# Performance work log

Measured on AMD Instinct MI355X. Metric: run time of the kernel, lower is better.

Reference implementation:

```python
import jax, jax.numpy as jnp
import numpy as np

H = 32; W = 32; KH = 3; KW = 3; NH = 8; DIM = 256; MLP_DIM = 1024; B = 4; T_FULL = 9
DH = DIM // NH
NEG = -1e9


def layernorm(x, g, b):
    m = jnp.mean(x, axis=-1, keepdims=True)
    v = jnp.var(x, axis=-1, keepdims=True)
    return (x - m) / jnp.sqrt(v + 1e-5) * g + b


def rope(x):
    # x: (B, NH, T, DH); split-half rotary position embedding
    T, dh = x.shape[-2], x.shape[-1]
    inv = 1.0 / (10000.0 ** (jnp.arange(0, dh, 2, dtype=jnp.float32) / dh))
    ang = jnp.arange(T, dtype=jnp.float32)[:, None] * inv  # (T, dh/2)
    cos, sin = jnp.cos(ang), jnp.sin(ang)
    x1, x2 = jnp.split(x, 2, axis=-1)
    return jnp.concatenate([x1 * cos - x2 * sin, x1 * sin + x2 * cos], axis=-1)


def setup_inputs() -> dict:
    key = jax.random.key(0)
    ks = jax.random.split(key, 16)
    def w(i, shp):
        return jax.random.normal(ks[i], shp, jnp.float32) * 0.02
    d = {
        'query': jax.random.normal(ks[0], (B, T_FULL, H * W, DIM), jnp.float32),
        'spatial_mask': jnp.zeros((1,), bool),          # unused by forward (module builds its own)
        'temporal_mask': jnp.zeros((T_FULL, T_FULL), bool),
        'sln_g': jnp.ones((DIM,), jnp.float32), 'sln_b': jnp.zeros((DIM,), jnp.float32),
        's_wq': w(1, (DIM, DIM)), 's_bq': jnp.zeros((DIM,), jnp.float32),
        's_wk': w(2, (DIM, DIM)), 's_bk': jnp.zeros((DIM,), jnp.float32),
        's_wv': w(3, (DIM, DIM)), 's_bv': jnp.zeros((DIM,), jnp.float32),
        's_wo': w(4, (DIM, DIM)), 's_bo': jnp.zeros((DIM,), jnp.float32),
        'tln_g': jnp.ones((DIM,), jnp.float32), 'tln_b': jnp.zeros((DIM,), jnp.float32),
        't_wq': w(5, (DIM, DIM)), 't_bq': jnp.zeros((DIM,), jnp.float32),
        't_wk': w(6, (DIM, DIM)), 't_bk': jnp.zeros((DIM,), jnp.float32),
        't_wv': w(7, (DIM, DIM)), 't_bv': jnp.zeros((DIM,), jnp.float32),
        't_wo': w(8, (DIM, DIM)), 't_bo': jnp.zeros((DIM,), jnp.float32),
        'mln_g': jnp.ones((DIM,), jnp.float32), 'mln_b': jnp.zeros((DIM,), jnp.float32),
        'w1': w(9, (DIM, MLP_DIM)), 'b1': jnp.zeros((MLP_DIM,), jnp.float32),
        'w2': w(10, (MLP_DIM, DIM)), 'b2': jnp.zeros((DIM,), jnp.float32),
    }
    return d


def _forward(query, temporal_mask, sln_g, sln_b, s_wq, s_bq, s_wk, s_bk, s_wv, s_bv, s_wo, s_bo,
             tln_g, tln_b, t_wq, t_bq, t_wk, t_bk, t_wv, t_bv, t_wo, t_bo,
             mln_g, mln_b, w1, b1, w2, b2):
    Bq, Tq, HWn, Dn = query.shape
    T = Tq - 1
    size = KH * KW
    scale = 1.0 / jnp.sqrt(jnp.float32(DH))

    # ---- spatial windowed attention on frames [:-1] (unfold -> per-window 1x9 attention) ----
    visual = query[:, :T].reshape(Bq * T, H, W, Dn)
    pad = jnp.pad(visual, ((0, 0), (KH // 2, KH // 2), (KW // 2, KW // 2), (0, 0)))
    neigh = jnp.stack([pad[:, i:i + H, j:j + W, :] for i in range(KH) for j in range(KW)], axis=1)
    neigh = neigh.reshape(Bq * T, size, HWn, Dn).transpose(0, 2, 1, 3)  # (BT, HW, size, D)
    onep = jnp.pad(jnp.ones((H, W), jnp.float32), ((KH // 2, KH // 2), (KW // 2, KW // 2)))
    valid = jnp.stack([onep[i:i + H, j:j + W] for i in range(KH) for j in range(KW)], axis=0)
    pad_mask = (valid.reshape(size, HWn).T == 0)  # (HW, size) True where neighbor from padding

    vis = visual.reshape(Bq * T, HWn, 1, Dn)
    vis_n = layernorm(vis, sln_g, sln_b)
    nei_n = layernorm(neigh, sln_g, sln_b)
    q = (vis_n @ s_wq + s_bq).reshape(Bq * T, HWn, 1, NH, DH)
    k = (nei_n @ s_wk + s_bk).reshape(Bq * T, HWn, size, NH, DH)
    v = (nei_n @ s_wv + s_bv).reshape(Bq * T, HWn, size, NH, DH)
    scores = jnp.einsum('bnqhd,bnkhd->bnhqk', q, k) * scale
    scores = jnp.where(pad_mask[None, :, None, None, :], NEG, scores)
    attn = jax.nn.softmax(scores, axis=-1)
    o = jnp.einsum('bnhqk,bnkhd->bnqhd', attn, v).reshape(Bq * T, HWn, 1, Dn)
    o = o @ s_wo + s_bo
    x_sp = (o + vis).reshape(Bq, T, HWn, Dn)

    x = jnp.concatenate([x_sp, query[:, -1:]], axis=1)  # (B, T_, HW, D)

    # ---- temporal RoPE attention per spatial location ----
    xt = x.transpose(0, 2, 1, 3).reshape(Bq * HWn, Tq, Dn)
    xn = layernorm(xt, tln_g, tln_b)
    qt = rope((xn @ t_wq + t_bq).reshape(-1, Tq, NH, DH).transpose(0, 2, 1, 3))
    kt = rope((xn @ t_wk + t_bk).reshape(-1, Tq, NH, DH).transpose(0, 2, 1, 3))
    vt = (xn @ t_wv + t_bv).reshape(-1, Tq, NH, DH).transpose(0, 2, 1, 3)
    sc = jnp.einsum('bhqd,bhkd->bhqk', qt, kt) * scale
    sc = jnp.where(temporal_mask[None, None, :, :], NEG, sc)
    at = jax.nn.softmax(sc, axis=-1)
    ot = jnp.einsum('bhqk,bhkd->bhqd', at, vt).transpose(0, 2, 1, 3).reshape(-1, Tq, Dn)
    xt = (ot @ t_wo + t_bo) + xt
    x = xt.reshape(Bq, HWn, Tq, Dn).transpose(0, 2, 1, 3)

    # CLS frame (t=0): average over spatial positions, broadcast back
    avg_cls = jnp.mean(x[:, 0], axis=1, keepdims=True)  # (B, 1, D)
    x = x.at[:, 0].set(jnp.broadcast_to(avg_cls, (Bq, HWn, Dn)))

    # ---- MLP block ----
    xm = layernorm(x, mln_g, mln_b)
    xm = jax.nn.gelu(xm @ w1 + b1, approximate=False) @ w2 + b2
    return xm + x


def reference(query, spatial_mask, temporal_mask, sln_g, sln_b, s_wq, s_bq, s_wk, s_bk, s_wv, s_bv, s_wo, s_bo, tln_g, tln_b, t_wq, t_bq, t_wk, t_bk, t_wv, t_bv, t_wo, t_bo, mln_g, mln_b, w1, b1, w2, b2):
    # spatial_mask is accepted but unused by the original forward (it rebuilds its own)
    return _forward(query, temporal_mask, sln_g, sln_b, s_wq, s_bq, s_wk, s_bk, s_wv, s_bv, s_wo, s_bo,
                    tln_g, tln_b, t_wq, t_bq, t_wk, t_bk, t_wv, t_bv, t_wo, t_bo,
                    mln_g, mln_b, w1, b1, w2, b2)
```

## Files before the change

### kernel.cpp

```cpp
#include <hip/hip_runtime.h>
#include <math.h>

#define TQ_  9

typedef unsigned int   u32;
typedef unsigned short ushort_t;
typedef short bf16x8 __attribute__((ext_vector_type(8)));
typedef float f32x4  __attribute__((ext_vector_type(4)));

__device__ __forceinline__ float bs2f(ushort_t s) {
  return __uint_as_float(((u32)s) << 16);
}
__device__ __forceinline__ ushort_t f2bs(float x) {
  u32 u = __float_as_uint(x);
  u32 r = (u + 0x7FFFu + ((u >> 16) & 1u)) >> 16;
  return (ushort_t)r;
}

struct TPA { const float* s[10]; ushort_t* d[10]; int K[10]; int N[10]; int pm[10]; };

__global__ __launch_bounds__(256)
void pack_all_kernel(TPA p) {
  int z = blockIdx.z;
  int K = p.K[z], N = p.N[z];
  int bn = blockIdx.x << 5, bk = blockIdx.y << 5;
  if (bn >= N || bk >= K) return;
  const float* W = p.s[z];
  ushort_t* pk = p.d[z];
  int pm = p.pm[z];
  __shared__ float t[32][33];
  int tid = threadIdx.x;
  int tx = tid & 31, ty = tid >> 5;
  #pragma unroll
  for (int r = 0; r < 4; ++r)
    t[ty + (r << 3)][tx] = W[(long)(bk + ty + (r << 3)) * N + bn + tx];
  __syncthreads();
  if (tid < 128) {
    int jl = tid >> 6, q = (tid >> 4) & 3, ln = tid & 15;
    int j = (bn >> 4) + jl, kk = bk >> 5;
    int colsrc = pm ? ((ln & 7) + (jl << 3) + ((ln & 8) << 1))
                    : ((jl << 4) + ln);
    long G = (((long)j * (K >> 5) + kk) << 6) + (q << 4) + ln;
    bf16x8 ov;
    #pragma unroll
    for (int e = 0; e < 8; ++e)
      ov[e] = (short)f2bs(t[(q << 3) + e][colsrc]);
    *(bf16x8*)(pk + (G << 3)) = ov;
  }
}

struct BC6 { const float* b[6]; };
__global__ __launch_bounds__(768)
void bias_concat_kernel(BC6 p, float* __restrict__ dst) {
  int z = blockIdx.x, n = threadIdx.x;
  int w = n >> 8, q = n & 255;
  int psrc = q;
  if (w < 2)
    psrc = (q & 0xE0) | (q & 7) | (((q >> 4) & 1) << 3) | (((q >> 3) & 1) << 4);
  dst[z * 768 + n] = p.b[z * 3 + w][psrc];
}

__global__ __launch_bounds__(256)
void ln_norm_kernel(const float* __restrict__ src, int spatial,
                    const float* __restrict__ g, const float* __restrict__ b,
                    ushort_t* __restrict__ dst) {
  int row = blockIdx.x * 4 + (threadIdx.x >> 6);
  int lane = threadIdx.x & 63;
  long srow = row;
  if (spatial) {
    int bq = row >> 13, r = row & 8191;
    srow = ((long)(bq * TQ_ + (r >> 10)) << 10) + (r & 1023);
  }
  float4 v = ((const float4*)(src + srow * 256))[lane];
  float s  = v.x + v.y + v.z + v.w;
  float s2 = v.x * v.x + v.y * v.y + v.z * v.z + v.w * v.w;
  #pragma unroll
  for (int m = 32; m; m >>= 1) {
    s  += __shfl_xor(s,  m, 64);
    s2 += __shfl_xor(s2, m, 64);
  }
  float mean = s * (1.f / 256.f);
  float rstd = rsqrtf(s2 * (1.f / 256.f) - mean * mean + 1e-5f);
  float4 gv = ((const float4*)g)[lane];
  float4 bv = ((const float4*)b)[lane];
  ushort_t o[4];
  o[0] = f2bs((v.x - mean) * rstd * gv.x + bv.x);
  o[1] = f2bs((v.y - mean) * rstd * gv.y + bv.y);
  o[2] = f2bs((v.z - mean) * rstd * gv.z + bv.z);
  o[3] = f2bs((v.w - mean) * rstd * gv.w + bv.w);
  u32 lo = (u32)o[0] | ((u32)o[1] << 16);
  u32 hi = (u32)o[2] | ((u32)o[3] << 16);
  uint2 pk; pk.x = lo; pk.y = hi;
  *(uint2*)(dst + (long)row * 256 + lane * 4) = pk;
}

template<int K>
__global__ __launch_bounds__(256, 4)
void wgemm_kernel(const ushort_t* __restrict__ A, int lda,
                  const ushort_t* __restrict__ packW,
                  const float* __restrict__ bias, const float* __restrict__ resid,
                  float* __restrict__ Cf, ushort_t* __restrict__ Cb,
                  int N, int NBq, int resid_mode, int out_mode, int act, int rope) {
  constexpr int K32 = K / 32;
  constexpr int AD = (K32 >= 4) ? 4 : K32;
  constexpr int BD = 2;

  int tid = threadIdx.x;
  int wv = tid >> 6, lane = tid & 63;
  int ln = lane & 15, q4 = lane >> 4;

  int gid = blockIdx.x;
  int g = gid >> 5, r = gid & 31;
  int nq = (r >> 3) + ((g % NBq) << 2);
  int mb = ((g / NBq) << 3) + (r & 7);
  int m0 = mb << 7, n0 = nq << 6;

  const ushort_t* Ap = A + (long)(m0 + (wv << 5) + ln) * lda + (q4 << 3);
  long a16 = (long)lda << 4;
  const ushort_t* Bp = packW + (((long)(nq << 2) * K32) << 9) + (lane << 3);

  bf16x8 xr[AD][2];
  bf16x8 wr[BD][4];
  #pragma unroll
  for (int d = 0; d < BD; ++d)
    #pragma unroll
    for (int j = 0; j < 4; ++j)
      wr[d][j] = *(const bf16x8*)(Bp + (((long)j * K32 + d) << 9));
  #pragma unroll
  for (int d = 0; d < AD; ++d) {
    xr[d][0] = *(const bf16x8*)(Ap + d * 32);
    xr[d][1] = *(const bf16x8*)(Ap + a16 + d * 32);
  }

  f32x4 acc[2][4];
  #pragma unroll
  for (int i = 0; i < 2; ++i)
    #pragma unroll
    for (int j = 0; j < 4; ++j) acc[i][j] = 0.f;

  #pragma unroll
  for (int kk = 0; kk < K32; ++kk) {
    #pragma unroll
    for (int i = 0; i < 2; ++i)
      #pragma unroll
      for (int j = 0; j < 4; ++j)
        acc[i][j] = __builtin_amdgcn_mfma_f32_16x16x32_bf16(
            wr[kk % BD][j], xr[kk % AD][i], acc[i][j], 0, 0, 0);
    if (kk + AD < K32) {
      xr[kk % AD][0] = *(const bf16x8*)(Ap + (kk + AD) * 32);
      xr[kk % AD][1] = *(const bf16x8*)(Ap + a16 + (kk + AD) * 32);
    }
    if (kk + BD < K32) {
      #pragma unroll
      for (int j = 0; j < 4; ++j)
        wr[kk % BD][j] = *(const bf16x8*)(Bp + (((long)j * K32 + kk + BD) << 9));
    }
    __builtin_amdgcn_sched_barrier(0);
  }

  float4 bj[4];
  #pragma unroll
  for (int j = 0; j < 4; ++j)
    bj[j] = *(const float4*)(bias + n0 + (j << 4) + (q4 << 2));

  float cs_c[2][4], cs_s[2][4];
  if (rope) {
    int t = (m0 >> 10) % TQ_;
    #pragma unroll
    for (int p = 0; p < 2; ++p)
      #pragma unroll
      for (int r2 = 0; r2 < 4; ++r2) {
        float d = (float)(((q4 & 1) << 2) + r2 + (p << 3));
        float ang = (float)t * exp2f(d * -0.8304820237218406f);
        cs_c[p][r2] = cosf(ang);
        float s = sinf(ang);
        cs_s[p][r2] = (q4 & 2) ? s : -s;
      }
  }

  #pragma unroll
  for (int i = 0; i < 2; ++i) {
    int m = m0 + (wv << 5) + (i << 4) + ln;
    long orow = m;
    if (out_mode == 1 || resid_mode == 2) {
      int bq = m >> 13, rr = m & 8191;
      orow = ((long)(bq * TQ_ + (rr >> 10)) << 10) + (rr & 1023);
    }
    #pragma unroll
    for (int j = 0; j < 4; ++j) {
      int n = n0 + (j << 4) + (q4 << 2);
      float v[4];
      #pragma unroll
      for (int r2 = 0; r2 < 4; ++r2) v[r2] = acc[i][j][r2] + bj[j][r2];
      if (rope && ((nq << 2) + j) < 32) {
        #pragma unroll
        for (int r2 = 0; r2 < 4; ++r2) {
          float other = __shfl_xor(v[r2], 32, 64);
          v[r2] = v[r2] * cs_c[j & 1][r2] + other * cs_s[j & 1][r2];
        }
      }
      if (act) {
        #pragma unroll
        for (int r2 = 0; r2 < 4; ++r2) {
          float x = v[r2];
          v[r2] = 0.5f * x * (1.f + erff(x * 0.70710678118654752f));
        }
      }
      if (resid_mode == 1) {
        float4 rv = *(const float4*)(resid + (long)m * 256 + n);
        v[0] += rv.x; v[1] += rv.y; v[2] += rv.z; v[3] += rv.w;
      } else if (resid_mode == 2) {
        float4 rv = *(const float4*)(resid + orow * 256 + n);
        v[0] += rv.x; v[1] += rv.y; v[2] += rv.z; v[3] += rv.w;
      }
      if (out_mode == 2) {
        uint2 pk;
        pk.x = (u32)f2bs(v[0]) | ((u32)f2bs(v[1]) << 16);
        pk.y = (u32)f2bs(v[2]) | ((u32)f2bs(v[3]) << 16);
        *(uint2*)(Cb + (long)m * N + n) = pk;
      } else {
        float4 o4; o4.x = v[0]; o4.y = v[1]; o4.z = v[2]; o4.w = v[3];
        if (out_mode == 1) *(float4*)(Cf + orow * 256 + n) = o4;
        else               *(float4*)(Cf + (long)m * N + n) = o4;
      }
    }
  }
}

__global__ __launch_bounds__(256)
void spatial_attn_kernel(ushort_t* __restrict__ qkv) {
  int gid = blockIdx.x * 256 + threadIdx.x;
  int head = gid & 7, pixel = gid >> 3;
  int pix = pixel & 1023, bt = pixel >> 10;
  int y = pix >> 5, x = pix & 31;
  long rb = (long)bt << 10;
  const float scale = 0.17677669529663687f;

  float qf[32];
  long qoff = (long)pixel * 768 + head * 32;
  #pragma unroll
  for (int i = 0; i < 4; ++i) {
    bf16x8 t = *(const bf16x8*)(qkv + qoff + i * 8);
    #pragma unroll
    for (int e = 0; e < 8; ++e) qf[i * 8 + e] = bs2f((ushort_t)t[e]);
  }

  float s[9];
  bool val[9];
  #pragma unroll
  for (int n = 0; n < 9; ++n) {
    int yy = y + n / 3 - 1, xx = x + n % 3 - 1;
    bool ok = ((unsigned)yy < 32u) & ((unsigned)xx < 32u);
    val[n] = ok;
    float d = 0.f;
    if (ok) {
      long ko = (rb + (yy << 5) + xx) * 768 + 256 + head * 32;
      #pragma unroll
      for (int i = 0; i < 4; ++i) {
        bf16x8 t = *(const bf16x8*)(qkv + ko + i * 8);
        #pragma unroll
        for (int e = 0; e < 8; ++e) d += qf[i * 8 + e] * bs2f((ushort_t)t[e]);
      }
    }
    s[n] = d * scale;
  }
  float mx = -1e30f;
  #pragma unroll
  for (int n = 0; n < 9; ++n) if (val[n]) mx = fmaxf(mx, s[n]);
  float sum = 0.f;
  #pragma unroll
  for (int n = 0; n < 9; ++n) { s[n] = val[n] ? __expf(s[n] - mx) : 0.f; sum += s[n]; }
  float inv = 1.f / sum;

  float o[32];
  #pragma unroll
  for (int i = 0; i < 32; ++i) o[i] = 0.f;
  #pragma unroll
  for (int n = 0; n < 9; ++n) {
    if (val[n]) {
      int yy = y + n / 3 - 1, xx = x + n % 3 - 1;
      long vo = (rb + (yy << 5) + xx) * 768 + 512 + head * 32;
      #pragma unroll
      for (int i = 0; i < 4; ++i) {
        bf16x8 t = *(const bf16x8*)(qkv + vo + i * 8);
        #pragma unroll
        for (int e = 0; e < 8; ++e) o[i * 8 + e] += s[n] * bs2f((ushort_t)t[e]);
      }
    }
  }
  #pragma unroll
  for (int i = 0; i < 4; ++i) {
    bf16x8 t;
    #pragma unroll
    for (int e = 0; e < 8; ++e) t[e] = (short)f2bs(o[i * 8 + e] * inv);
    *(bf16x8*)(qkv + qoff + i * 8) = t;
  }
}

__global__ __launch_bounds__(256)
void temporal_attn_kernel(ushort_t* __restrict__ qkv) {
  int tid = threadIdx.x;
  int head = tid & 7, hwi = tid >> 3;
  int bi = blockIdx.x;
  int tq = bi >> 7;
  int rest = bi & 127;
  int b = rest >> 5, hwg = rest & 31;
  int hw = (hwg << 5) + hwi;
  long base = (long)(b * TQ_) * 1024 + hw;
  const float scale = 0.17677669529663687f;

  float qf[32];
  long qoff = (base + (long)tq * 1024) * 768 + head * 32;
  #pragma unroll
  for (int i = 0; i < 4; ++i) {
    bf16x8 t = *(const bf16x8*)(qkv + qoff + i * 8);
    #pragma unroll
    for (int e = 0; e < 8; ++e) qf[i * 8 + e] = bs2f((ushort_t)t[e]);
  }
  float s[9];
  #pragma unroll
  for (int tk = 0; tk < 9; ++tk) {
    long ko = (base + (long)tk * 1024) * 768 + 256 + head * 32;
    float d = 0.f;
    #pragma unroll
    for (int i = 0; i < 4; ++i) {
      bf16x8 t = *(const bf16x8*)(qkv + ko + i * 8);
      #pragma unroll
      for (int e = 0; e < 8; ++e) d += qf[i * 8 + e] * bs2f((ushort_t)t[e]);
    }
    s[tk] = d * scale;
  }
  float mx = s[0];
  #pragma unroll
  for (int tk = 1; tk < 9; ++tk) mx = fmaxf(mx, s[tk]);
  float sum = 0.f;
  #pragma unroll
  for (int tk = 0; tk < 9; ++tk) { s[tk] = __expf(s[tk] - mx); sum += s[tk]; }
  float inv = 1.f / sum;

  float o[32];
  #pragma unroll
  for (int i = 0; i < 32; ++i) o[i] = 0.f;
  #pragma unroll
  for (int tk = 0; tk < 9; ++tk) {
    long vo = (base + (long)tk * 1024) * 768 + 512 + head * 32;
    #pragma unroll
    for (int i = 0; i < 4; ++i) {
      bf16x8 t = *(const bf16x8*)(qkv + vo + i * 8);
      #pragma unroll
      for (int e = 0; e < 8; ++e) o[i * 8 + e] += s[tk] * bs2f((ushort_t)t[e]);
    }
  }
  #pragma unroll
  for (int i = 0; i < 4; ++i) {
    bf16x8 t;
    #pragma unroll
    for (int e = 0; e < 8; ++e) t[e] = (short)f2bs(o[i * 8 + e] * inv);
    *(bf16x8*)(qkv + qoff + i * 8) = t;
  }
}

__global__ __launch_bounds__(256)
void copy_frame8_kernel(const float* __restrict__ qy, float* __restrict__ x) {
  long i = (long)blockIdx.x * 256 + threadIdx.x;
  int b = (int)(i >> 18);
  long rem = i & ((1L << 18) - 1);
  long gi = ((long)(b * TQ_ + 8) << 18) + rem;
  x[gi] = qy[gi];
}

__global__ __launch_bounds__(256)
void cls_sum_kernel(const float* __restrict__ x, float* __restrict__ partial) {
  int b = blockIdx.x >> 5, ch = blockIdx.x & 31;
  int d = threadIdx.x;
  long base = ((long)(b * TQ_) * 1024 + ch * 32) * 256 + d;
  float s = 0.f;
  for (int r = 0; r < 32; ++r) s += x[base + (long)r * 256];
  partial[(long)blockIdx.x * 256 + d] = s;
}

__global__ __launch_bounds__(256)
void cls_bcast_kernel(float* __restrict__ x, const float* __restrict__ partial) {
  int b = blockIdx.x >> 3, seg = blockIdx.x & 7;
  int d = threadIdx.x;
  float s = 0.f;
  for (int j = 0; j < 32; ++j) s += partial[(long)(b * 32 + j) * 256 + d];
  s *= (1.f / 1024.f);
  long base = ((long)(b * TQ_) * 1024 + seg * 128) * 256 + d;
  for (int r = 0; r < 128; ++r) x[base + (long)r * 256] = s;
}

extern "C" void kernel_launch(void* const* d_in, const int* in_sizes, int n_in,
                              void* d_out, int out_size, void* d_ws, size_t ws_size,
                              hipStream_t stream) {
  (void)in_sizes; (void)n_in; (void)out_size; (void)ws_size;
  const float* query = (const float*)d_in[0];
  const float* sln_g = (const float*)d_in[3];
  const float* sln_b = (const float*)d_in[4];
  const float* s_wq  = (const float*)d_in[5];
  const float* s_bq  = (const float*)d_in[6];
  const float* s_wk  = (const float*)d_in[7];
  const float* s_bk  = (const float*)d_in[8];
  const float* s_wv  = (const float*)d_in[9];
  const float* s_bv  = (const float*)d_in[10];
  const float* s_wo  = (const float*)d_in[11];
  const float* s_bo  = (const float*)d_in[12];
  const float* tln_g = (const float*)d_in[13];
  const float* tln_b = (const float*)d_in[14];
  const float* t_wq  = (const float*)d_in[15];
  const float* t_bq  = (const float*)d_in[16];
  const float* t_wk  = (const float*)d_in[17];
  const float* t_bk  = (const float*)d_in[18];
  const float* t_wv  = (const float*)d_in[19];
  const float* t_bv  = (const float*)d_in[20];
  const float* t_wo  = (const float*)d_in[21];
  const float* t_bo  = (const float*)d_in[22];
  const float* mln_g = (const float*)d_in[23];
  const float* mln_b = (const float*)d_in[24];
  const float* w1    = (const float*)d_in[25];
  const float* b1    = (const float*)d_in[26];
  const float* w2    = (const float*)d_in[27];
  const float* b2    = (const float*)d_in[28];
  float* out = (float*)d_out;

  const long RB = 36864L * 256;
  ushort_t* XA  = (ushort_t*)d_ws;
  ushort_t* QKV = XA + RB;
  float*    P4  = (float*)(QKV + 3 * RB);
  ushort_t* wt  = (ushort_t*)(P4 + RB);
  float* bias2  = (float*)(wt + 1048576);
  float* clsp   = bias2 + 1536;
  ushort_t* hid = QKV;

  ushort_t* pk_sqkv = wt;
  ushort_t* pk_tqkv = wt + 196608;
  ushort_t* pk_swo  = wt + 393216;
  ushort_t* pk_two  = wt + 458752;
  ushort_t* pk_w1   = wt + 524288;
  ushort_t* pk_w2   = wt + 786432;

  TPA tp;
  tp.s[0] = s_wq; tp.d[0] = pk_sqkv;          tp.K[0] = 256;  tp.N[0] = 256;  tp.pm[0] = 1;
  tp.s[1] = s_wk; tp.d[1] = pk_sqkv + 65536;  tp.K[1] = 256;  tp.N[1] = 256;  tp.pm[1] = 1;
  tp.s[2] = s_wv; tp.d[2] = pk_sqkv + 131072; tp.K[2] = 256;  tp.N[2] = 256;  tp.pm[2] = 0;
  tp.s[3] = t_wq; tp.d[3] = pk_tqkv;          tp.K[3] = 256;  tp.N[3] = 256;  tp.pm[3] = 1;
  tp.s[4] = t_wk; tp.d[4] = pk_tqkv + 65536;  tp.K[4] = 256;  tp.N[4] = 256;  tp.pm[4] = 1;
  tp.s[5] = t_wv; tp.d[5] = pk_tqkv + 131072; tp.K[5] = 256;  tp.N[5] = 256;  tp.pm[5] = 0;
  tp.s[6] = s_wo; tp.d[6] = pk_swo;           tp.K[6] = 256;  tp.N[6] = 256;  tp.pm[6] = 0;
  tp.s[7] = t_wo; tp.d[7] = pk_two;           tp.K[7] = 256;  tp.N[7] = 256;  tp.pm[7] = 0;
  tp.s[8] = w1;   tp.d[8] = pk_w1;            tp.K[8] = 256;  tp.N[8] = 1024; tp.pm[8] = 0;
  tp.s[9] = w2;   tp.d[9] = pk_w2;            tp.K[9] = 1024; tp.N[9] = 256;  tp.pm[9] = 0;
  pack_all_kernel<<<dim3(32, 32, 10), 256, 0, stream>>>(tp);
  BC6 bc;
  bc.b[0] = s_bq; bc.b[1] = s_bk; bc.b[2] = s_bv;
  bc.b[3] = t_bq; bc.b[4] = t_bk; bc.b[5] = t_bv;
  bias_concat_kernel<<<2, 768, 0, stream>>>(bc, bias2);

  #define WGEMM(KV, Ap, ldav, Wp, bi, rs, CF, CB, M, N, rm, om, ac, rp)     \
    wgemm_kernel<KV><<<dim3(((M) / 128) * ((N) / 64)), 256, 0, stream>>>(   \
        Ap, ldav, Wp, bi, rs, CF, CB, N, (N) / 256, rm, om, ac, rp)

  ln_norm_kernel<<<8192, 256, 0, stream>>>(query, 1, sln_g, sln_b, XA);
  WGEMM(256, XA, 256, pk_sqkv, bias2, nullptr, nullptr, QKV,
        32768, 768, 0, 2, 0, 0);
  spatial_attn_kernel<<<1024, 256, 0, stream>>>(QKV);
  WGEMM(256, QKV, 768, pk_swo, s_bo, query, P4, nullptr,
        32768, 256, 2, 1, 0, 0);
  copy_frame8_kernel<<<4096, 256, 0, stream>>>(query, P4);

  ln_norm_kernel<<<9216, 256, 0, stream>>>(P4, 0, tln_g, tln_b, XA);
  WGEMM(256, XA, 256, pk_tqkv, bias2 + 768, nullptr, nullptr, QKV,
        36864, 768, 0, 2, 0, 1);
  temporal_attn_kernel<<<1152, 256, 0, stream>>>(QKV);
  WGEMM(256, QKV, 768, pk_two, t_bo, P4, out, nullptr,
        36864, 256, 1, 0, 0, 0);

  cls_sum_kernel<<<128, 256, 0, stream>>>(out, clsp);
  cls_bcast_kernel<<<32, 256, 0, stream>>>(out, clsp);

  ln_norm_kernel<<<9216, 256, 0, stream>>>(out, 0, mln_g, mln_b, XA);
  WGEMM(256, XA, 256, pk_w1, b1, nullptr, nullptr, hid,
        36864, 1024, 0, 2, 1, 0);
  WGEMM(1024, hid, 1024, pk_w2, b2, out, out, nullptr,
        36864, 256, 1, 0, 0, 0);
  #undef WGEMM
}
```

Before: 527.1 us.

## Fuse MLP LayerNorm, W1 GEMM, GELU and W2 GEMM into one kernel

Replaces the separate LayerNorm, W1 GEMM (writing a 36864x1024 bf16 hidden buffer) and W2 GEMM with a single kernel. Each 64-thread block handles 32 rows: it normalizes them into LDS, computes the hidden activations in 64-column chunks with GELU, and immediately accumulates them into the W2 output using MFMA. This removes the global round trip of the large hidden tensor. In exchange, each single-wave block streams all of W1 and W2 from global or cache without LDS reuse, and occupancy is low at 1152 one-wave blocks.

```diff
diff --git a/kernel.cpp b/kernel.cpp
--- a/kernel.cpp
+++ b/kernel.cpp
@@ -223,6 +223,148 @@
         if (out_mode == 1) *(float4*)(Cf + orow * 256 + n) = o4;
         else               *(float4*)(Cf + (long)m * N + n) = o4;
       }
+    }
+  }
+}
+
+__device__ __forceinline__ int xl_off(int row, int col) {
+  return (row << 8) + (((((col >> 3) + row) & 31)) << 3) + (col & 7);
+}
+__device__ __forceinline__ int hl_off(int row, int col) {
+  return (row << 6) + (((((col >> 3) + row) & 7)) << 3) + (col & 7);
+}
+
+__global__ __launch_bounds__(64)
+void mlp_fused_kernel(float* xio,
+                      const ushort_t* __restrict__ W1p,
+                      const float* __restrict__ b1,
+                      const ushort_t* __restrict__ W2p,
+                      const float* __restrict__ b2,
+                      const float* __restrict__ g,
+                      const float* __restrict__ be) {
+  __shared__ ushort_t XL[8192];
+  __shared__ ushort_t HL[2048];
+  int lane = threadIdx.x;
+  int ln = lane & 15, q4 = lane >> 4;
+  int m0 = blockIdx.x << 5;
+
+  float mean[2], rstd[2];
+  #pragma unroll
+  for (int i = 0; i < 2; ++i) {
+    const float* xr = xio + (long)(m0 + (i << 4) + ln) * 256 + (q4 << 3);
+    float s = 0.f, s2 = 0.f;
+    #pragma unroll
+    for (int ks = 0; ks < 8; ++ks) {
+      float4 a = *(const float4*)(xr + (ks << 5));
+      float4 b = *(const float4*)(xr + (ks << 5) + 4);
+      s  += a.x + a.y + a.z + a.w + b.x + b.y + b.z + b.w;
+      s2 += a.x*a.x + a.y*a.y + a.z*a.z + a.w*a.w
+          + b.x*b.x + b.y*b.y + b.z*b.z + b.w*b.w;
+    }
+    s  += __shfl_xor(s,  16, 64);  s  += __shfl_xor(s,  32, 64);
+    s2 += __shfl_xor(s2, 16, 64);  s2 += __shfl_xor(s2, 32, 64);
+    mean[i] = s * (1.f / 256.f);
+    rstd[i] = rsqrtf(s2 * (1.f / 256.f) - mean[i] * mean[i] + 1e-5f);
+  }
+
+  #pragma unroll
+  for (int ks = 0; ks < 8; ++ks) {
+    int col = (q4 << 3) + (ks << 5);
+    float4 ga = *(const float4*)(g + col);
+    float4 gb = *(const float4*)(g + col + 4);
+    float4 ba = *(const float4*)(be + col);
+    float4 bb = *(const float4*)(be + col + 4);
+    #pragma unroll
+    for (int i = 0; i < 2; ++i) {
+      const float* xr = xio + (long)(m0 + (i << 4) + ln) * 256 + col;
+      float4 a = *(const float4*)(xr);
+      float4 b = *(const float4*)(xr + 4);
+      float m_ = mean[i], r_ = rstd[i];
+      u32 w0 = (u32)f2bs((a.x - m_) * r_ * ga.x + ba.x)
+             | ((u32)f2bs((a.y - m_) * r_ * ga.y + ba.y) << 16);
+      u32 w1_ = (u32)f2bs((a.z - m_) * r_ * ga.z + ba.z)
+             | ((u32)f2bs((a.w - m_) * r_ * ga.w + ba.w) << 16);
+      u32 w2_ = (u32)f2bs((b.x - m_) * r_ * gb.x + bb.x)
+             | ((u32)f2bs((b.y - m_) * r_ * gb.y + bb.y) << 16);
+      u32 w3 = (u32)f2bs((b.z - m_) * r_ * gb.z + bb.z)
+             | ((u32)f2bs((b.w - m_) * r_ * gb.w + bb.w) << 16);
+      uint4 pk; pk.x = w0; pk.y = w1_; pk.z = w2_; pk.w = w3;
+      *(uint4*)&XL[xl_off((i << 4) + ln, col)] = pk;
+    }
+  }
+
+  f32x4 acc[2][16];
+  #pragma unroll
+  for (int i = 0; i < 2; ++i)
+    #pragma unroll
+    for (int jo = 0; jo < 16; ++jo) acc[i][jo] = 0.f;
+
+  #pragma unroll 1
+  for (int c = 0; c < 16; ++c) {
+    f32x4 h[2][4];
+    #pragma unroll
+    for (int i = 0; i < 2; ++i)
+      #pragma unroll
+      for (int jj = 0; jj < 4; ++jj) h[i][jj] = 0.f;
+
+    #pragma unroll
+    for (int ks = 0; ks < 8; ++ks) {
+      int col = (q4 << 3) + (ks << 5);
+      bf16x8 xf0 = *(const bf16x8*)&XL[xl_off(ln, col)];
+      bf16x8 xf1 = *(const bf16x8*)&XL[xl_off(16 + ln, col)];
+      #pragma unroll
+      for (int jj = 0; jj < 4; ++jj) {
+        bf16x8 wf = *(const bf16x8*)(W1p +
+            (((long)((c << 2) + jj) * 8 + ks) << 9) + (lane << 3));
+        h[0][jj] = __builtin_amdgcn_mfma_f32_16x16x32_bf16(wf, xf0, h[0][jj], 0, 0, 0);
+        h[1][jj] = __builtin_amdgcn_mfma_f32_16x16x32_bf16(wf, xf1, h[1][jj], 0, 0, 0);
+      }
+    }
+    #pragma unroll
+    for (int jj = 0; jj < 4; ++jj) {
+      float4 b1v = *(const float4*)(b1 + (c << 6) + (jj << 4) + (q4 << 2));
+      #pragma unroll
+      for (int i = 0; i < 2; ++i) {
+        float v[4];
+        v[0] = h[i][jj][0] + b1v.x;  v[1] = h[i][jj][1] + b1v.y;
+        v[2] = h[i][jj][2] + b1v.z;  v[3] = h[i][jj][3] + b1v.w;
+        #pragma unroll
+        for (int r = 0; r < 4; ++r)
+          v[r] = 0.5f * v[r] * (1.f + erff(v[r] * 0.70710678118654752f));
+        uint2 pk;
+        pk.x = (u32)f2bs(v[0]) | ((u32)f2bs(v[1]) << 16);
+        pk.y = (u32)f2bs(v[2]) | ((u32)f2bs(v[3]) << 16);
+        *(uint2*)&HL[hl_off((i << 4) + ln, (jj << 4) + (q4 << 2))] = pk;
+      }
+    }
+    #pragma unroll
+    for (int ks2 = 0; ks2 < 2; ++ks2) {
+      bf16x8 hb0 = *(const bf16x8*)&HL[hl_off(ln,      (ks2 << 5) + (q4 << 3))];
+      bf16x8 hb1 = *(const bf16x8*)&HL[hl_off(16 + ln, (ks2 << 5) + (q4 << 3))];
+      #pragma unroll
+      for (int jo = 0; jo < 16; ++jo) {
+        bf16x8 wf = *(const bf16x8*)(W2p +
+            (((long)(jo << 5) + (c << 1) + ks2) << 9) + (lane << 3));
+        acc[0][jo] = __builtin_amdgcn_mfma_f32_16x16x32_bf16(wf, hb0, acc[0][jo], 0, 0, 0);
+        acc[1][jo] = __builtin_amdgcn_mfma_f32_16x16x32_bf16(wf, hb1, acc[1][jo], 0, 0, 0);
+      }
+    }
+  }
+
+  #pragma unroll
+  for (int i = 0; i < 2; ++i) {
+    long ro = (long)(m0 + (i << 4) + ln) * 256;
+    #pragma unroll
+    for (int jo = 0; jo < 16; ++jo) {
+      int colb = (jo << 4) + (q4 << 2);
+      float4 rv = *(const float4*)(xio + ro + colb);
+      float4 bv = *(const float4*)(b2 + colb);
+      float4 o;
+      o.x = acc[i][jo][0] + bv.x + rv.x;
+      o.y = acc[i][jo][1] + bv.y + rv.y;
+      o.z = acc[i][jo][2] + bv.z + rv.z;
+      o.w = acc[i][jo][3] + bv.w + rv.w;
+      *(float4*)(xio + ro + colb) = o;
     }
   }
 }
@@ -430,7 +572,6 @@
   ushort_t* wt  = (ushort_t*)(P4 + RB);
   float* bias2  = (float*)(wt + 1048576);
   float* clsp   = bias2 + 1536;
-  ushort_t* hid = QKV;
 
   ushort_t* pk_sqkv = wt;
   ushort_t* pk_tqkv = wt + 196608;
@@ -478,10 +619,7 @@
   cls_sum_kernel<<<128, 256, 0, stream>>>(out, clsp);
   cls_bcast_kernel<<<32, 256, 0, stream>>>(out, clsp);
 
-  ln_norm_kernel<<<9216, 256, 0, stream>>>(out, 0, mln_g, mln_b, XA);
-  WGEMM(256, XA, 256, pk_w1, b1, nullptr, nullptr, hid,
-        36864, 1024, 0, 2, 1, 0);
-  WGEMM(1024, hid, 1024, pk_w2, b2, out, out, nullptr,
-        36864, 256, 1, 0, 0, 0);
+  mlp_fused_kernel<<<1152, 64, 0, stream>>>(out, pk_w1, b1, pk_w2, b2,
+                                            mln_g, mln_b);
   #undef WGEMM
 }
```

Result: slower. 983.8 us (+86.6%).
